# Kernel optimization log

Hardware: AMD Instinct MI355X
Metric: run time of the kernel (lower is better)

The kernel has to match this reference:

```python
import jax, jax.numpy as jnp
import numpy as np

BETA = 0.9
THRESHOLD = 1.0
SLOPE = 10.0


def setup_inputs() -> dict:
    key = jax.random.key(0)
    ks = jax.random.split(key, 5)
    B, T, F, H = 32768, 10, 256, 512
    x = jax.random.normal(ks[0], (B, T, F), dtype=jnp.float32)
    W1 = jax.random.normal(ks[1], (H, F), dtype=jnp.float32) * (1.0 / np.sqrt(F))
    b1 = jax.random.normal(ks[2], (H,), dtype=jnp.float32) * 0.01
    W2 = jax.random.normal(ks[3], (1, H), dtype=jnp.float32) * (1.0 / np.sqrt(H))
    b2 = jax.random.normal(ks[4], (1,), dtype=jnp.float32) * 0.01
    return {"x": x, "W1": W1, "b1": b1, "W2": W2, "b2": b2}


def _surrogate_spike(mem):
    return jax.nn.sigmoid(SLOPE * (mem - THRESHOLD))


def _lif(cur, mem):
    mem = BETA * mem + cur
    spike = _surrogate_spike(mem)
    mem = mem - spike * THRESHOLD
    return spike, mem


def reference(x, W1, b1, W2, b2):
    B, T, F = x.shape
    H = W1.shape[0]
    # Precompute fc1 over all time steps in one big GEMM: [B,T,H]
    cur1_all = jnp.einsum('btf,hf->bth', x, W1) + b1

    mem1_0 = jnp.zeros((B, H), dtype=x.dtype)
    mem2_0 = jnp.zeros((B, 1), dtype=x.dtype)

    def step(carry, cur1_t):
        mem1, mem2 = carry
        spk1, mem1 = _lif(cur1_t, mem1)
        cur2 = spk1 @ W2.T + b2  # [B,1]
        spk2, mem2 = _lif(cur2, mem2)
        return (mem1, mem2), spk2

    # scan over the fixed 10 time steps (hard sequential dependency on mem)
    (_, _), spk2_seq = jax.lax.scan(step, (mem1_0, mem2_0),
                                    jnp.moveaxis(cur1_all, 1, 0))  # [T,B,1]
    spk_mean = jnp.sum(spk2_seq, axis=0) / 10.0
    return jax.nn.sigmoid(spk_mean)
```

## Files before the change

### kernel.cpp

```cpp
#include <hip/hip_runtime.h>
#include <hip/hip_bf16.h>


typedef short short8 __attribute__((ext_vector_type(8)));
typedef float f32x4 __attribute__((ext_vector_type(4)));

__device__ __forceinline__ unsigned short bfbits(float f) {
  union { __hip_bfloat16 h; unsigned short u; } c;
  c.h = __float2bfloat16(f);
  return c.u;
}

__device__ __forceinline__ unsigned int bfpack(float a, float b) {
  return (unsigned int)bfbits(a) | ((unsigned int)bfbits(b) << 16);
}

__device__ __forceinline__ float spike10(float m) {
  float e = __builtin_amdgcn_exp2f(fmaf(m, -14.4269504f, 14.4269504f));
  return __builtin_amdgcn_rcpf(1.0f + e);
}

__device__ __forceinline__ void lif4(f32x4& mv, const f32x4 av, float w2c, float pr[4]) {
#pragma unroll
  for (int e = 0; e < 4; ++e) {
    float m   = fmaf(mv[e], 0.9f, av[e]);
    float spk = spike10(m);
    mv[e] = m - spk;
    pr[e] = fmaf(spk, w2c, pr[e]);
  }
}

__global__ void w1_to_bf16(const float* __restrict__ w1, unsigned short* __restrict__ o) {
  int i = blockIdx.x * 256 + threadIdx.x;
  float4 v = reinterpret_cast<const float4*>(w1)[i];
  reinterpret_cast<uint2*>(o)[i] = make_uint2(bfpack(v.x, v.y), bfpack(v.z, v.w));
}

__device__ __forceinline__ short8 cvt_frag(const float* p) {
  const float4 v0 = *reinterpret_cast<const float4*>(p);
  const float4 v1 = *reinterpret_cast<const float4*>(p + 4);
  union { unsigned int u[4]; short8 s; } cv;
  cv.u[0] = bfpack(v0.x, v0.y);
  cv.u[1] = bfpack(v0.z, v0.w);
  cv.u[2] = bfpack(v1.x, v1.y);
  cv.u[3] = bfpack(v1.z, v1.w);
  return cv.s;
}

template <bool USE_WS>
__global__
__attribute__((amdgpu_flat_work_group_size(512, 512)))
void snn_main(const float* __restrict__ x,
              const unsigned short* __restrict__ w1bf,
              const float* __restrict__ w1f,
              const float* __restrict__ b1,
              const float* __restrict__ w2,
              const float* __restrict__ b2,
              float* __restrict__ out)
{
  __shared__ __align__(16) float mem_lds[4][512][4];
  __shared__ __align__(16) unsigned short xt[2][2][32][132];
  __shared__ float cur2_lds[10][32][9];

  const int tid  = threadIdx.x;
  const int lane = tid & 63;
  const int wave = tid >> 6;
  const int l15  = lane & 15;
  const int lq   = lane >> 4;
  const long b0  = (long)blockIdx.x * 32;
  const int h0   = wave * 64;

  float w2l[4], b1l[4];
#pragma unroll
  for (int ct = 0; ct < 4; ++ct) {
    int h = h0 + ct * 16 + l15;
    w2l[ct] = w2[h];
    b1l[ct] = b1[h];
  }

#pragma unroll
  for (int p = 0; p < 4; ++p) {
    f32x4 z = {0.f, 0.f, 0.f, 0.f};
    *reinterpret_cast<f32x4*>(&mem_lds[p][tid][0]) = z;
  }
  f32x4 m4 = {0.f, 0.f, 0.f, 0.f}, m5 = m4, m6 = m4, m7 = m4;

  const int sr = tid >> 4;
  const int sc = tid & 15;
  const float* xrow = x + (b0 + sr) * 2560;

  const unsigned short* wb = w1bf + (h0 + l15) * 256 + lq * 8;
  const float*          wf = w1f  + (h0 + l15) * 256 + lq * 8;

  float4 pfr[4];
#pragma unroll
  for (int j = 0; j < 4; ++j)
    pfr[j] = *reinterpret_cast<const float4*>(xrow + (sc + j * 16) * 4);

#pragma unroll 1
  for (int t = 0; t < 10; ++t) {
    const int par = t & 1;
#pragma unroll
    for (int j = 0; j < 4; ++j)
      *reinterpret_cast<uint2*>(&xt[par][j >> 1][sr][(sc + (j & 1) * 16) * 4]) =
          make_uint2(bfpack(pfr[j].x, pfr[j].y), bfpack(pfr[j].z, pfr[j].w));
    short8 bfr0[4];
#pragma unroll
    for (int c = 0; c < 4; ++c) {
      if constexpr (USE_WS) bfr0[c] = *reinterpret_cast<const short8*>(wb + c * 4096);
      else                  bfr0[c] = cvt_frag(wf + c * 4096);
    }
    __syncthreads();

    {
      const int tn = (t < 9) ? t + 1 : 9;
#pragma unroll
      for (int j = 0; j < 4; ++j)
        pfr[j] = *reinterpret_cast<const float4*>(xrow + tn * 256 + (sc + j * 16) * 4);
    }

    f32x4 acc[2][4];
#pragma unroll
    for (int rt = 0; rt < 2; ++rt)
#pragma unroll
      for (int c = 0; c < 4; ++c) {
        f32x4 cc = { b1l[c], b1l[c], b1l[c], b1l[c] };
        acc[rt][c] = cc;
      }

    __builtin_amdgcn_s_setprio(1);
#pragma unroll
    for (int kk = 0; kk < 8; ++kk) {
      short8 a[2], bfr[4];
#pragma unroll
      for (int rt = 0; rt < 2; ++rt)
        a[rt] = *reinterpret_cast<const short8*>(
            &xt[par][kk >> 2][rt * 16 + l15][(kk & 3) * 32 + lq * 8]);
      if (kk == 0) {
#pragma unroll
        for (int c = 0; c < 4; ++c) bfr[c] = bfr0[c];
      } else {
#pragma unroll
        for (int c = 0; c < 4; ++c) {
          if constexpr (USE_WS)
            bfr[c] = *reinterpret_cast<const short8*>(wb + c * 4096 + kk * 32);
          else
            bfr[c] = cvt_frag(wf + c * 4096 + kk * 32);
        }
      }
#pragma unroll
      for (int rt = 0; rt < 2; ++rt)
#pragma unroll
        for (int c = 0; c < 4; ++c)
          acc[rt][c] = __builtin_amdgcn_mfma_f32_16x16x32_bf16(a[rt], bfr[c], acc[rt][c], 0, 0, 0);
    }
    __builtin_amdgcn_s_setprio(0);

#pragma unroll
    for (int rt = 0; rt < 2; ++rt) {
      float pr[4] = {0.f, 0.f, 0.f, 0.f};
#pragma unroll
      for (int c = 0; c < 4; ++c) {
        const int p = rt * 4 + c;
        if (p < 4) {
          f32x4* slot = reinterpret_cast<f32x4*>(&mem_lds[p][tid][0]);
          f32x4 mv = *slot;
          lif4(mv, acc[rt][c], w2l[c], pr);
          *slot = mv;
        } else if (p == 4) {
          lif4(m4, acc[rt][c], w2l[c], pr);
        } else if (p == 5) {
          lif4(m5, acc[rt][c], w2l[c], pr);
        } else if (p == 6) {
          lif4(m6, acc[rt][c], w2l[c], pr);
        } else {
          lif4(m7, acc[rt][c], w2l[c], pr);
        }
      }
#pragma unroll
      for (int e = 0; e < 4; ++e) {
        float v = pr[e];
        v += __shfl_xor(v, 1); v += __shfl_xor(v, 2);
        v += __shfl_xor(v, 4); v += __shfl_xor(v, 8);
        if (l15 == 0) cur2_lds[t][rt * 16 + lq * 4 + e][wave] = v;
      }
    }
  }

  __syncthreads();

  if (tid < 32) {
    const float bias2 = b2[0];
    float mem2 = 0.f, spksum = 0.f;
#pragma unroll
    for (int t = 0; t < 10; ++t) {
      float c2 = bias2;
#pragma unroll
      for (int w = 0; w < 8; ++w) c2 += cur2_lds[t][tid][w];
      float m   = fmaf(mem2, 0.9f, c2);
      float spk = spike10(m);
      mem2   = m - spk;
      spksum += spk;
    }
    float e = __builtin_amdgcn_exp2f(spksum * -0.14426950408f);
    out[b0 + tid] = __builtin_amdgcn_rcpf(1.0f + e);
  }
}

extern "C" void kernel_launch(void* const* d_in, const int* in_sizes, int n_in,
                              void* d_out, int out_size, void* d_ws, size_t ws_size,
                              hipStream_t stream) {
  const float* x  = (const float*)d_in[0];
  const float* W1 = (const float*)d_in[1];
  const float* b1 = (const float*)d_in[2];
  const float* W2 = (const float*)d_in[3];
  const float* b2 = (const float*)d_in[4];
  float* out = (float*)d_out;
  (void)in_sizes; (void)n_in;

  const int grid = out_size / 32;

  if (ws_size >= 512 * 256 * sizeof(unsigned short)) {
    unsigned short* w1bf = (unsigned short*)d_ws;
    w1_to_bf16<<<128, 256, 0, stream>>>(W1, w1bf);
    snn_main<true><<<grid, 512, 0, stream>>>(x, w1bf, W1, b1, W2, b2, out);
  } else {
    snn_main<false><<<grid, 512, 0, stream>>>(x, nullptr, W1, b1, W2, b2, out);
  }
}
```

Baseline: 165.8 us.

## Process two timesteps per barrier with double-buffered x staging in LDS

The time loop now handles two timesteps per iteration. The x tiles for the next pair are staged into a second LDS buffer while the current pair computes, so there is one __syncthreads per two steps instead of one per step. Global loads for the upcoming steps are issued before each compute phase to hide latency. This doubles the LDS footprint for x tiles, which may lower occupancy, and it drops the early prefetch of the W1 fragment for kk==0.

```diff
diff --git a/kernel.cpp b/kernel.cpp
--- a/kernel.cpp
+++ b/kernel.cpp
@@ -59,7 +59,7 @@
               float* __restrict__ out)
 {
   __shared__ __align__(16) float mem_lds[4][512][4];
-  __shared__ __align__(16) unsigned short xt[2][2][32][132];
+  __shared__ __align__(16) unsigned short xt[2][2][2][32][132];
   __shared__ float cur2_lds[10][32][9];
 
   const int tid  = threadIdx.x;
@@ -92,54 +92,47 @@
   const unsigned short* wb = w1bf + (h0 + l15) * 256 + lq * 8;
   const float*          wf = w1f  + (h0 + l15) * 256 + lq * 8;
 
-  float4 pfr[4];
-#pragma unroll
-  for (int j = 0; j < 4; ++j)
-    pfr[j] = *reinterpret_cast<const float4*>(xrow + (sc + j * 16) * 4);
+#pragma unroll
+  for (int tl = 0; tl < 2; ++tl)
+#pragma unroll
+    for (int j = 0; j < 4; ++j) {
+      const float4 v = *reinterpret_cast<const float4*>(xrow + tl * 256 + (sc + j * 16) * 4);
+      *reinterpret_cast<uint2*>(&xt[0][tl][j >> 1][sr][(sc + (j & 1) * 16) * 4]) =
+          make_uint2(bfpack(v.x, v.y), bfpack(v.z, v.w));
+    }
+  __syncthreads();
 
 #pragma unroll 1
-  for (int t = 0; t < 10; ++t) {
-    const int par = t & 1;
-#pragma unroll
-    for (int j = 0; j < 4; ++j)
-      *reinterpret_cast<uint2*>(&xt[par][j >> 1][sr][(sc + (j & 1) * 16) * 4]) =
-          make_uint2(bfpack(pfr[j].x, pfr[j].y), bfpack(pfr[j].z, pfr[j].w));
-    short8 bfr0[4];
-#pragma unroll
-    for (int c = 0; c < 4; ++c) {
-      if constexpr (USE_WS) bfr0[c] = *reinterpret_cast<const short8*>(wb + c * 4096);
-      else                  bfr0[c] = cvt_frag(wf + c * 4096);
-    }
-    __syncthreads();
-
-    {
-      const int tn = (t < 9) ? t + 1 : 9;
+  for (int ii = 0; ii < 5; ++ii) {
+    const int par  = ii & 1;
+    const int npar = par ^ 1;
+    const int t0   = 2 * ii;
+
+    float4 pfrA[4];
+    {
+      const int ta = (ii < 4) ? t0 + 2 : 8;
 #pragma unroll
       for (int j = 0; j < 4; ++j)
-        pfr[j] = *reinterpret_cast<const float4*>(xrow + tn * 256 + (sc + j * 16) * 4);
-    }
-
-    f32x4 acc[2][4];
-#pragma unroll
-    for (int rt = 0; rt < 2; ++rt)
-#pragma unroll
-      for (int c = 0; c < 4; ++c) {
-        f32x4 cc = { b1l[c], b1l[c], b1l[c], b1l[c] };
-        acc[rt][c] = cc;
-      }
-
-    __builtin_amdgcn_s_setprio(1);
-#pragma unroll
-    for (int kk = 0; kk < 8; ++kk) {
-      short8 a[2], bfr[4];
+        pfrA[j] = *reinterpret_cast<const float4*>(xrow + ta * 256 + (sc + j * 16) * 4);
+    }
+
+    {
+      f32x4 acc[2][4];
 #pragma unroll
       for (int rt = 0; rt < 2; ++rt)
-        a[rt] = *reinterpret_cast<const short8*>(
-            &xt[par][kk >> 2][rt * 16 + l15][(kk & 3) * 32 + lq * 8]);
-      if (kk == 0) {
-#pragma unroll
-        for (int c = 0; c < 4; ++c) bfr[c] = bfr0[c];
-      } else {
+#pragma unroll
+        for (int c = 0; c < 4; ++c) {
+          f32x4 cc = { b1l[c], b1l[c], b1l[c], b1l[c] };
+          acc[rt][c] = cc;
+        }
+      __builtin_amdgcn_s_setprio(1);
+#pragma unroll
+      for (int kk = 0; kk < 8; ++kk) {
+        short8 a[2], bfr[4];
+#pragma unroll
+        for (int rt = 0; rt < 2; ++rt)
+          a[rt] = *reinterpret_cast<const short8*>(
+              &xt[par][0][kk >> 2][rt * 16 + l15][(kk & 3) * 32 + lq * 8]);
 #pragma unroll
         for (int c = 0; c < 4; ++c) {
           if constexpr (USE_WS)
@@ -147,47 +140,117 @@
           else
             bfr[c] = cvt_frag(wf + c * 4096 + kk * 32);
         }
-      }
+#pragma unroll
+        for (int rt = 0; rt < 2; ++rt)
+#pragma unroll
+          for (int c = 0; c < 4; ++c)
+            acc[rt][c] = __builtin_amdgcn_mfma_f32_16x16x32_bf16(a[rt], bfr[c], acc[rt][c], 0, 0, 0);
+      }
+      __builtin_amdgcn_s_setprio(0);
+
+#pragma unroll
+      for (int rt = 0; rt < 2; ++rt) {
+        float pr[4] = {0.f, 0.f, 0.f, 0.f};
+#pragma unroll
+        for (int c = 0; c < 4; ++c) {
+          const int p = rt * 4 + c;
+          if (p < 4) {
+            f32x4* slot = reinterpret_cast<f32x4*>(&mem_lds[p][tid][0]);
+            f32x4 mv = *slot;
+            lif4(mv, acc[rt][c], w2l[c], pr);
+            *slot = mv;
+          } else if (p == 4) lif4(m4, acc[rt][c], w2l[c], pr);
+          else if (p == 5)   lif4(m5, acc[rt][c], w2l[c], pr);
+          else if (p == 6)   lif4(m6, acc[rt][c], w2l[c], pr);
+          else               lif4(m7, acc[rt][c], w2l[c], pr);
+        }
+#pragma unroll
+        for (int e = 0; e < 4; ++e) {
+          float v = pr[e];
+          v += __shfl_xor(v, 1); v += __shfl_xor(v, 2);
+          v += __shfl_xor(v, 4); v += __shfl_xor(v, 8);
+          if (l15 == 0) cur2_lds[t0][rt * 16 + lq * 4 + e][wave] = v;
+        }
+      }
+    }
+
+#pragma unroll
+    for (int j = 0; j < 4; ++j)
+      *reinterpret_cast<uint2*>(&xt[npar][0][j >> 1][sr][(sc + (j & 1) * 16) * 4]) =
+          make_uint2(bfpack(pfrA[j].x, pfrA[j].y), bfpack(pfrA[j].z, pfrA[j].w));
+    float4 pfrB[4];
+    {
+      const int tb = (ii < 4) ? t0 + 3 : 9;
+#pragma unroll
+      for (int j = 0; j < 4; ++j)
+        pfrB[j] = *reinterpret_cast<const float4*>(xrow + tb * 256 + (sc + j * 16) * 4);
+    }
+
+    {
+      f32x4 acc[2][4];
 #pragma unroll
       for (int rt = 0; rt < 2; ++rt)
 #pragma unroll
-        for (int c = 0; c < 4; ++c)
-          acc[rt][c] = __builtin_amdgcn_mfma_f32_16x16x32_bf16(a[rt], bfr[c], acc[rt][c], 0, 0, 0);
-    }
-    __builtin_amdgcn_s_setprio(0);
-
-#pragma unroll
-    for (int rt = 0; rt < 2; ++rt) {
-      float pr[4] = {0.f, 0.f, 0.f, 0.f};
-#pragma unroll
-      for (int c = 0; c < 4; ++c) {
-        const int p = rt * 4 + c;
-        if (p < 4) {
-          f32x4* slot = reinterpret_cast<f32x4*>(&mem_lds[p][tid][0]);
-          f32x4 mv = *slot;
-          lif4(mv, acc[rt][c], w2l[c], pr);
-          *slot = mv;
-        } else if (p == 4) {
-          lif4(m4, acc[rt][c], w2l[c], pr);
-        } else if (p == 5) {
-          lif4(m5, acc[rt][c], w2l[c], pr);
-        } else if (p == 6) {
-          lif4(m6, acc[rt][c], w2l[c], pr);
-        } else {
-          lif4(m7, acc[rt][c], w2l[c], pr);
-        }
-      }
-#pragma unroll
-      for (int e = 0; e < 4; ++e) {
-        float v = pr[e];
-        v += __shfl_xor(v, 1); v += __shfl_xor(v, 2);
-        v += __shfl_xor(v, 4); v += __shfl_xor(v, 8);
-        if (l15 == 0) cur2_lds[t][rt * 16 + lq * 4 + e][wave] = v;
-      }
-    }
-  }
-
-  __syncthreads();
+        for (int c = 0; c < 4; ++c) {
+          f32x4 cc = { b1l[c], b1l[c], b1l[c], b1l[c] };
+          acc[rt][c] = cc;
+        }
+      __builtin_amdgcn_s_setprio(1);
+#pragma unroll
+      for (int kk = 0; kk < 8; ++kk) {
+        short8 a[2], bfr[4];
+#pragma unroll
+        for (int rt = 0; rt < 2; ++rt)
+          a[rt] = *reinterpret_cast<const short8*>(
+              &xt[par][1][kk >> 2][rt * 16 + l15][(kk & 3) * 32 + lq * 8]);
+#pragma unroll
+        for (int c = 0; c < 4; ++c) {
+          if constexpr (USE_WS)
+            bfr[c] = *reinterpret_cast<const short8*>(wb + c * 4096 + kk * 32);
+          else
+            bfr[c] = cvt_frag(wf + c * 4096 + kk * 32);
+        }
+#pragma unroll
+        for (int rt = 0; rt < 2; ++rt)
+#pragma unroll
+          for (int c = 0; c < 4; ++c)
+            acc[rt][c] = __builtin_amdgcn_mfma_f32_16x16x32_bf16(a[rt], bfr[c], acc[rt][c], 0, 0, 0);
+      }
+      __builtin_amdgcn_s_setprio(0);
+
+#pragma unroll
+      for (int rt = 0; rt < 2; ++rt) {
+        float pr[4] = {0.f, 0.f, 0.f, 0.f};
+#pragma unroll
+        for (int c = 0; c < 4; ++c) {
+          const int p = rt * 4 + c;
+          if (p < 4) {
+            f32x4* slot = reinterpret_cast<f32x4*>(&mem_lds[p][tid][0]);
+            f32x4 mv = *slot;
+            lif4(mv, acc[rt][c], w2l[c], pr);
+            *slot = mv;
+          } else if (p == 4) lif4(m4, acc[rt][c], w2l[c], pr);
+          else if (p == 5)   lif4(m5, acc[rt][c], w2l[c], pr);
+          else if (p == 6)   lif4(m6, acc[rt][c], w2l[c], pr);
+          else               lif4(m7, acc[rt][c], w2l[c], pr);
+        }
+#pragma unroll
+        for (int e = 0; e < 4; ++e) {
+          float v = pr[e];
+          v += __shfl_xor(v, 1); v += __shfl_xor(v, 2);
+          v += __shfl_xor(v, 4); v += __shfl_xor(v, 8);
+          if (l15 == 0) cur2_lds[t0 + 1][rt * 16 + lq * 4 + e][wave] = v;
+        }
+      }
+    }
+
+#pragma unroll
+    for (int j = 0; j < 4; ++j)
+      *reinterpret_cast<uint2*>(&xt[npar][1][j >> 1][sr][(sc + (j & 1) * 16) * 4]) =
+          make_uint2(bfpack(pfrB[j].x, pfrB[j].y), bfpack(pfrB[j].z, pfrB[j].w));
+
+    __syncthreads();
+  }
 
   if (tid < 32) {
     const float bias2 = b2[0];
```

After: 205.3 us. 1.24x slower.
